# Kernel tuning notes

Hardware: AMD Instinct MI355X
Metric: run time of the kernel (lower is better)

The kernel has to match this reference:

```python
import jax, jax.numpy as jnp
import numpy as np

B, S, D, H = 2, 2048, 1024, 16
DK = D // H
NEG = -1.0e9


def setup_inputs() -> dict:
    key = jax.random.key(0)
    ks = jax.random.split(key, 11)
    inp = {
        "q": jax.random.normal(ks[0], (B, S, D), jnp.float32),
        "k": jax.random.normal(ks[1], (B, S, D), jnp.float32),
        "v": jax.random.normal(ks[2], (B, S, D), jnp.float32),
        "mask": jnp.tril(jnp.ones((S, S), jnp.int32))[None, None],  # causal [1,1,S,S]
    }
    scale = 0.02
    inp["w_q"] = jax.random.normal(ks[3], (D, D), jnp.float32) * scale
    inp["b_q"] = jnp.zeros((D,), jnp.float32)
    inp["w_k"] = jax.random.normal(ks[4], (D, D), jnp.float32) * scale
    inp["b_k"] = jnp.zeros((D,), jnp.float32)
    inp["w_v"] = jax.random.normal(ks[5], (D, D), jnp.float32) * scale
    inp["b_v"] = jnp.zeros((D,), jnp.float32)
    inp["w_o"] = jax.random.normal(ks[6], (D, D), jnp.float32) * scale
    inp["b_o"] = jnp.zeros((D,), jnp.float32)
    return inp


def reference(q, k, v, mask, w_q, b_q, w_k, b_k, w_v, b_v, w_o, b_o):
    # projections: [B,S,D] -> [B,H,S,DK]
    def proj(x, w, b):
        y = jnp.einsum("bsd,de->bse", x, w) + b
        return y.reshape(B, S, H, DK).transpose(0, 2, 1, 3)

    Q = proj(q, w_q, b_q)
    K = proj(k, w_k, b_k)
    V = proj(v, w_v, b_v)
    # explicit scores matrix, faithful to the original naive attention
    scores = jnp.einsum("bhsd,bhtd->bhst", Q, K) / jnp.sqrt(jnp.float32(DK))
    scores = jnp.where(mask == 0, NEG, scores)
    attn = jax.nn.softmax(scores, axis=-1)  # dropout p=0.0 -> identity
    x = jnp.einsum("bhst,bhtd->bhsd", attn, V)
    x = x.transpose(0, 2, 1, 3).reshape(B, S, D)
    return jnp.einsum("bsd,de->bse", x, w_o) + b_o
```

## Files before the change

### kernel.cpp

```cpp
#include <hip/hip_runtime.h>
#include <hip/hip_bf16.h>

typedef __bf16 bf16;
typedef __bf16 bf16x2 __attribute__((ext_vector_type(2)));
typedef __bf16 bf16x8 __attribute__((ext_vector_type(8)));
typedef float f32x4 __attribute__((ext_vector_type(4)));

#define MFMA16(a, b, c) __builtin_amdgcn_mfma_f32_16x16x32_bf16(a, b, c, 0, 0, 0)

#define QSCALE 0.18033688f

__global__ __launch_bounds__(256) void convert_k(const float* __restrict__ q,
                                                 const float* __restrict__ k,
                                                 const float* __restrict__ v,
                                                 bf16* __restrict__ qb,
                                                 bf16* __restrict__ kb,
                                                 bf16* __restrict__ vb) {
  const float* src = blockIdx.y == 0 ? q : blockIdx.y == 1 ? k : v;
  bf16* dst = blockIdx.y == 0 ? qb : blockIdx.y == 1 ? kb : vb;
  const size_t i = ((size_t)blockIdx.x * 256 + threadIdx.x) * 8;
  float4 a = *(const float4*)(src + i);
  float4 b = *(const float4*)(src + i + 4);
  bf16x8 o;
  o[0] = (bf16)a.x; o[1] = (bf16)a.y; o[2] = (bf16)a.z; o[3] = (bf16)a.w;
  o[4] = (bf16)b.x; o[5] = (bf16)b.y; o[6] = (bf16)b.z; o[7] = (bf16)b.w;
  *(bf16x8*)(dst + i) = o;
}

__global__ __launch_bounds__(256) void transpose_w(const float* __restrict__ w0,
                                                   const float* __restrict__ w1,
                                                   const float* __restrict__ w2,
                                                   const float* __restrict__ w3,
                                                   bf16* __restrict__ dst) {
  __shared__ bf16 T[64][68];
  const float* W = blockIdx.z == 0 ? w0 : blockIdx.z == 1 ? w1
                   : blockIdx.z == 2 ? w2 : w3;
  bf16* Y = dst + (size_t)blockIdx.z * 1024 * 1024;
  const int t = threadIdx.x, r = t >> 2, c4 = t & 3;
  const int k0 = blockIdx.y * 64, n0 = blockIdx.x * 64;

  const float4* src = (const float4*)(W + (size_t)(k0 + r) * 1024 + n0 + c4 * 16);
  float4 f0 = src[0], f1 = src[1], f2 = src[2], f3 = src[3];
  bf16* row = &T[r][c4 * 16];
  row[0] = (bf16)f0.x; row[1] = (bf16)f0.y; row[2] = (bf16)f0.z; row[3] = (bf16)f0.w;
  row[4] = (bf16)f1.x; row[5] = (bf16)f1.y; row[6] = (bf16)f1.z; row[7] = (bf16)f1.w;
  row[8] = (bf16)f2.x; row[9] = (bf16)f2.y; row[10] = (bf16)f2.z; row[11] = (bf16)f2.w;
  row[12] = (bf16)f3.x; row[13] = (bf16)f3.y; row[14] = (bf16)f3.z; row[15] = (bf16)f3.w;
  __syncthreads();

  bf16x8 o0, o1;
#pragma unroll
  for (int j = 0; j < 8; ++j) o0[j] = T[c4 * 16 + j][r];
#pragma unroll
  for (int j = 0; j < 8; ++j) o1[j] = T[c4 * 16 + 8 + j][r];
  bf16* d = Y + (size_t)(n0 + r) * 1024 + k0 + c4 * 16;
  *(bf16x8*)d = o0;
  *(bf16x8*)(d + 8) = o1;
}

template <int QKV, int MT>
__global__ __launch_bounds__(256, 3) void gemm_p(
    const bf16* __restrict__ xq, const bf16* __restrict__ xk,
    const bf16* __restrict__ xv, const bf16* __restrict__ Wt,
    const float* __restrict__ bq, const float* __restrict__ bk,
    const float* __restrict__ bv, bf16* __restrict__ Qp,
    bf16* __restrict__ Kp, bf16* __restrict__ Vtp, float* __restrict__ Yf) {
  constexpr int AROWS = MT * 32;
  __shared__ bf16 Al[AROWS * 72];
  __shared__ bf16 Bl[128 * 72];

  const int z = QKV ? blockIdx.z : 0;
  const bf16* X = QKV ? (z == 0 ? xq : z == 1 ? xk : xv) : xq;
  const bf16* Bt = Wt + (size_t)z * 1048576;
  const float* bias = QKV ? (z == 0 ? bq : z == 1 ? bk : bv) : bq;
  const float escale = (QKV && z == 0) ? QSCALE : 1.0f;

  const int t = threadIdx.x;
  const int wave = t >> 6, lane = t & 63, quad = lane >> 4, l16 = lane & 15;
  const int wm = (wave >> 1) * (MT * 16), wn = (wave & 1) * 64;
  const int bm = blockIdx.y * AROWS, bn = blockIdx.x * 128;

  constexpr int NA = (MT == 4) ? 4 : 2;
  const int arow = (MT == 4) ? (t >> 1) : (t >> 2);
  const int acol = (MT == 4) ? ((t & 1) * 32) : ((t & 3) * 16);
  const int brow = t >> 1, bcol = (t & 1) * 32;
  const bf16* gA = X + (size_t)(bm + arow) * 1024 + acol;
  const bf16* gB = Bt + (size_t)(bn + brow) * 1024 + bcol;

  bf16x8 ra[NA], rb[4];
#pragma unroll
  for (int j = 0; j < NA; ++j) ra[j] = *(const bf16x8*)(gA + j * 8);
#pragma unroll
  for (int j = 0; j < 4; ++j) rb[j] = *(const bf16x8*)(gB + j * 8);

  f32x4 acc[MT][4] = {};

  for (int kb = 0; kb < 1024; kb += 64) {
    __syncthreads();
#pragma unroll
    for (int j = 0; j < NA; ++j)
      *(bf16x8*)(Al + arow * 72 + acol + j * 8) = ra[j];
#pragma unroll
    for (int j = 0; j < 4; ++j)
      *(bf16x8*)(Bl + brow * 72 + bcol + j * 8) = rb[j];
    __syncthreads();

    if (kb + 64 < 1024) {
#pragma unroll
      for (int j = 0; j < NA; ++j)
        ra[j] = *(const bf16x8*)(gA + kb + 64 + j * 8);
#pragma unroll
      for (int j = 0; j < 4; ++j)
        rb[j] = *(const bf16x8*)(gB + kb + 64 + j * 8);
    }

#pragma unroll
    for (int kk = 0; kk < 2; ++kk) {
      bf16x8 af[MT], bfr[4];
#pragma unroll
      for (int mt = 0; mt < MT; ++mt)
        af[mt] =
            *(const bf16x8*)(Al + (wm + mt * 16 + l16) * 72 + kk * 32 + quad * 8);
#pragma unroll
      for (int nt = 0; nt < 4; ++nt)
        bfr[nt] =
            *(const bf16x8*)(Bl + (wn + nt * 16 + l16) * 72 + kk * 32 + quad * 8);
#pragma unroll
      for (int mt = 0; mt < MT; ++mt)
#pragma unroll
        for (int nt = 0; nt < 4; ++nt)
          acc[mt][nt] = MFMA16(af[mt], bfr[nt], acc[mt][nt]);
    }
  }

  if (QKV && z == 2) {
    bf16* Tt = Al;
    const int b = bm >> 11;
    __syncthreads();
#pragma unroll
    for (int half = 0; half < 2; ++half) {
      if ((wave & 1) == half) {
#pragma unroll
        for (int nt = 0; nt < 4; ++nt) {
          const int ln = nt * 16 + l16;
          const float bia = bias[bn + half * 64 + ln];
#pragma unroll
          for (int mt = 0; mt < 4; ++mt)
#pragma unroll
            for (int r = 0; r < 4; ++r) {
              const int m = wm + mt * 16 + quad * 4 + r;
              Tt[ln * 136 + m] = (bf16)(acc[mt][nt][r] + bia);
            }
        }
      }
      __syncthreads();
      {
        const int ln = t >> 2, seg = (t & 3) * 32;
        const int gn = bn + half * 64 + ln;
        const int h = gn >> 6, dk = gn & 63;
        const int s0 = (bm & 2047) + seg;
        bf16* dstp = Vtp + ((size_t)(b * 16 + h) * 64 + dk) * 2048 + s0;
        const bf16* srcp = Tt + ln * 136 + seg;
#pragma unroll
        for (int j = 0; j < 4; ++j)
          *(bf16x8*)(dstp + j * 8) = *(const bf16x8*)(srcp + j * 8);
      }
      __syncthreads();
    }
  } else {
#pragma unroll
    for (int mt = 0; mt < MT; ++mt)
#pragma unroll
      for (int nt = 0; nt < 4; ++nt) {
        const int gn = bn + wn + nt * 16 + l16;
        const float bia = bias[gn];
#pragma unroll
        for (int r = 0; r < 4; ++r) {
          const int gm = bm + wm + mt * 16 + quad * 4 + r;
          const float val = (acc[mt][nt][r] + bia) * escale;
          if (!QKV) {
            Yf[(size_t)gm * 1024 + gn] = val;
          } else {
            const int b = gm >> 11, s = gm & 2047;
            const int h = gn >> 6, dk = gn & 63;
            bf16* Y = (z == 0) ? Qp : Kp;
            Y[((size_t)(b * 16 + h) * 2048 + s) * 64 + dk] = (bf16)val;
          }
        }
      }
  }
}

__global__ __launch_bounds__(256) void attn_k(const bf16* __restrict__ Q,
                                              const bf16* __restrict__ K,
                                              const bf16* __restrict__ Vt,
                                              bf16* __restrict__ X) {
  __shared__ bf16 Kl[64 * 72];
  __shared__ bf16 Vl[64 * 72];
  __shared__ bf16 Pb[4][16 * 72];

  const int t = threadIdx.x;
  const int wave = t >> 6, lane = t & 63, quad = lane >> 4, l16 = lane & 15;
  const int pairx = blockIdx.x, bh = blockIdx.y;
  const int b = bh >> 4, h = bh & 15;

  const bf16* Qb = Q + (size_t)bh * 2048 * 64;
  const bf16* Kb = K + (size_t)bh * 2048 * 64;
  const bf16* Vb = Vt + (size_t)bh * 64 * 2048;

  const int srow = t >> 2;
  const int scol = (t & 3) * 16;
  const int crow = (srow & 32) + ((srow & 1) << 4) + ((srow & 31) >> 1);

  bf16x8 onesf;
#pragma unroll
  for (int i = 0; i < 8; ++i) onesf[i] = (bf16)1.0f;

  bf16* Pw = Pb[wave];

  for (int phase = 0; phase < 2; ++phase) {
    const int qtile = phase ? (31 - pairx) : pairx;
    const int ntiles = qtile + 1;
    const int q0 = qtile * 64 + wave * 16;

    bf16x8 qf0 = *(const bf16x8*)(Qb + (q0 + l16) * 64 + quad * 8);
    bf16x8 qf1 = *(const bf16x8*)(Qb + (q0 + l16) * 64 + 32 + quad * 8);

    f32x4 o[4] = {};
    f32x4 o4 = {};

    {
      const bf16* kp = Kb + srow * 64 + scol;
      const bf16* vp = Vb + (size_t)srow * 2048 + scol;
      bf16x8 k0r = *(const bf16x8*)kp;
      bf16x8 k1r = *(const bf16x8*)(kp + 8);
      bf16x8 v0r = *(const bf16x8*)vp;
      bf16x8 v1r = *(const bf16x8*)(vp + 8);
      *(bf16x8*)(Kl + crow * 72 + scol) = k0r;
      *(bf16x8*)(Kl + crow * 72 + scol + 8) = k1r;
      *(bf16x8*)(Vl + srow * 72 + scol) = v0r;
      *(bf16x8*)(Vl + srow * 72 + scol + 8) = v1r;
    }
    __syncthreads();

    for (int kt = 0; kt < ntiles; ++kt) {
      const int k0 = kt * 64;
      const bool more = (kt + 1) < ntiles;
      bf16x8 kr0, kr1, vr0, vr1;
      if (more) {
        const bf16* kp = Kb + (k0 + 64 + srow) * 64 + scol;
        const bf16* vp = Vb + (size_t)srow * 2048 + k0 + 64 + scol;
        kr0 = *(const bf16x8*)kp;
        kr1 = *(const bf16x8*)(kp + 8);
        vr0 = *(const bf16x8*)vp;
        vr1 = *(const bf16x8*)(vp + 8);
      }

      f32x4 sc[4];
#pragma unroll
      for (int nt = 0; nt < 4; ++nt) {
        bf16x8 kf0 = *(const bf16x8*)(Kl + (nt * 16 + l16) * 72 + quad * 8);
        bf16x8 kf1 = *(const bf16x8*)(Kl + (nt * 16 + l16) * 72 + 32 + quad * 8);
        f32x4 s = {};
        s = MFMA16(qf0, kf0, s);
        s = MFMA16(qf1, kf1, s);
        sc[nt] = s;
      }

      const bool interior = (k0 + 63) <= q0;
#pragma unroll
      for (int r = 0; r < 4; ++r) {
        const int row = quad * 4 + r;
        float e0 = exp2f(sc[0][r]);
        float e1 = exp2f(sc[1][r]);
        float e2 = exp2f(sc[2][r]);
        float e3 = exp2f(sc[3][r]);
        if (!interior) {
          const int qg = q0 + row;
          const int key0 = k0 + 2 * l16;
          if (key0 > qg) e0 = 0.f;
          if (key0 + 1 > qg) e1 = 0.f;
          if (key0 + 32 > qg) e2 = 0.f;
          if (key0 + 33 > qg) e3 = 0.f;
        }
        bf16x2 p01, p23;
        p01[0] = (bf16)e0; p01[1] = (bf16)e1;
        p23[0] = (bf16)e2; p23[1] = (bf16)e3;
        *(bf16x2*)(Pw + row * 72 + 2 * l16) = p01;
        *(bf16x2*)(Pw + row * 72 + 32 + 2 * l16) = p23;
      }
      __builtin_amdgcn_s_waitcnt(0xC07F);

      bf16x8 pf0 = *(const bf16x8*)(Pw + l16 * 72 + quad * 8);
      bf16x8 pf1 = *(const bf16x8*)(Pw + l16 * 72 + 32 + quad * 8);
      o4 = MFMA16(pf0, onesf, o4);
      o4 = MFMA16(pf1, onesf, o4);
#pragma unroll
      for (int dt = 0; dt < 4; ++dt) {
        bf16x8 vf0 = *(const bf16x8*)(Vl + (dt * 16 + l16) * 72 + quad * 8);
        bf16x8 vf1 = *(const bf16x8*)(Vl + (dt * 16 + l16) * 72 + 32 + quad * 8);
        o[dt] = MFMA16(pf0, vf0, o[dt]);
        o[dt] = MFMA16(pf1, vf1, o[dt]);
      }

      __syncthreads();
      if (more) {
        *(bf16x8*)(Kl + crow * 72 + scol) = kr0;
        *(bf16x8*)(Kl + crow * 72 + scol + 8) = kr1;
        *(bf16x8*)(Vl + srow * 72 + scol) = vr0;
        *(bf16x8*)(Vl + srow * 72 + scol + 8) = vr1;
        __syncthreads();
      }
    }

#pragma unroll
    for (int r = 0; r < 4; ++r) {
      const float rinv = 1.0f / o4[r];
      const int qg = q0 + quad * 4 + r;
#pragma unroll
      for (int dt = 0; dt < 4; ++dt) {
        const int col = h * 64 + dt * 16 + l16;
        X[((size_t)b * 2048 + qg) * 1024 + col] = (bf16)(o[dt][r] * rinv);
      }
    }
    __syncthreads();
  }
}

extern "C" void kernel_launch(void* const* d_in, const int* in_sizes, int n_in,
                              void* d_out, int out_size, void* d_ws,
                              size_t ws_size, hipStream_t stream) {
  const float* q = (const float*)d_in[0];
  const float* k = (const float*)d_in[1];
  const float* v = (const float*)d_in[2];
  const float* w_q = (const float*)d_in[4];
  const float* b_q = (const float*)d_in[5];
  const float* w_k = (const float*)d_in[6];
  const float* b_k = (const float*)d_in[7];
  const float* w_v = (const float*)d_in[8];
  const float* b_v = (const float*)d_in[9];
  const float* w_o = (const float*)d_in[10];
  const float* b_o = (const float*)d_in[11];

  bf16* ws = (bf16*)d_ws;
  const size_t NELEM = (size_t)4096 * 1024;
  bf16* Qp = ws;
  bf16* Kp = ws + NELEM;
  bf16* Vtp = ws + 2 * NELEM;
  bf16* Xp = ws + 3 * NELEM;
  bf16* Wt = ws + 4 * NELEM;
  bf16* Wto = Wt + 3145728;
  bf16* qb = Xp;
  bf16* kb = (bf16*)d_out;
  bf16* vb = kb + NELEM;

  convert_k<<<dim3(2048, 3), 256, 0, stream>>>(q, k, v, qb, kb, vb);
  transpose_w<<<dim3(16, 16, 4), 256, 0, stream>>>(w_q, w_k, w_v, w_o, Wt);

  gemm_p<1, 4><<<dim3(8, 32, 3), 256, 0, stream>>>(
      qb, kb, vb, Wt, b_q, b_k, b_v, Qp, Kp, Vtp, nullptr);
  attn_k<<<dim3(16, 32), 256, 0, stream>>>(Qp, Kp, Vtp, Xp);
  gemm_p<0, 2><<<dim3(8, 64), 256, 0, stream>>>(
      Xp, nullptr, nullptr, Wto, b_o, nullptr, nullptr, nullptr, nullptr,
      nullptr, (float*)d_out);
}
```

Before: 244.3 us.

## Rewrite attention kernel with 32x32 MFMA, double-buffered swizzled LDS, register softmax

The attention kernel now gives each wave 32 query rows (128-row block tiles) and uses 32x32x16 bf16 MFMA with a transposed S=K*Q^T so P can be built in registers through cross-half shuffles. This replaces the LDS round-trip for P and the ones-vector MFMA used for row sums. K/V tiles are double-buffered in XOR-swizzled LDS so each iteration needs only one barrier. A 1D grid maps heads across XCDs and pairs short and long causal tiles for balance, with setprio around MFMA bursts. The costs are higher register pressure from two f32x16 accumulators and coarser causal tiles that do more masked work on the diagonal.

```diff
diff --git a/kernel.cpp b/kernel.cpp
--- a/kernel.cpp
+++ b/kernel.cpp
@@ -5,8 +5,10 @@
 typedef __bf16 bf16x2 __attribute__((ext_vector_type(2)));
 typedef __bf16 bf16x8 __attribute__((ext_vector_type(8)));
 typedef float f32x4 __attribute__((ext_vector_type(4)));
+typedef float f32x16 __attribute__((ext_vector_type(16)));
 
 #define MFMA16(a, b, c) __builtin_amdgcn_mfma_f32_16x16x32_bf16(a, b, c, 0, 0, 0)
+#define MFMA32(a, b, c) __builtin_amdgcn_mfma_f32_32x32x16_bf16(a, b, c, 0, 0, 0)
 
 #define QSCALE 0.18033688f
 
@@ -191,139 +193,165 @@
   }
 }
 
-__global__ __launch_bounds__(256) void attn_k(const bf16* __restrict__ Q,
-                                              const bf16* __restrict__ K,
-                                              const bf16* __restrict__ Vt,
-                                              bf16* __restrict__ X) {
-  __shared__ bf16 Kl[64 * 72];
-  __shared__ bf16 Vl[64 * 72];
-  __shared__ bf16 Pb[4][16 * 72];
+__global__ __launch_bounds__(256, 2) void attn_k(const bf16* __restrict__ Q,
+                                                 const bf16* __restrict__ K,
+                                                 const bf16* __restrict__ Vt,
+                                                 bf16* __restrict__ X) {
+  __shared__ __align__(16) bf16 Kl[2][64 * 64];
+  __shared__ __align__(16) bf16 Vl[2][64 * 64];
+  __shared__ float rsL[4][32];
 
   const int t = threadIdx.x;
-  const int wave = t >> 6, lane = t & 63, quad = lane >> 4, l16 = lane & 15;
-  const int pairx = blockIdx.x, bh = blockIdx.y;
-  const int b = bh >> 4, h = bh & 15;
+  const int wave = t >> 6, lane = t & 63;
+  const int cl = lane & 31, h = lane >> 5;
+
+  const int n = blockIdx.x;
+  const int xcd = n & 7, mm = n >> 3;
+  const int bh = xcd + 8 * (mm & 3);
+  const int ii = mm >> 2;
+  const int qt = (ii < 8) ? ii : 23 - ii;
+  const int ntiles = 2 * qt + 2;
+  const int q0 = qt * 128 + wave * 32;
+  const int b = bh >> 4, hh = bh & 15;
 
   const bf16* Qb = Q + (size_t)bh * 2048 * 64;
   const bf16* Kb = K + (size_t)bh * 2048 * 64;
   const bf16* Vb = Vt + (size_t)bh * 64 * 2048;
 
-  const int srow = t >> 2;
-  const int scol = (t & 3) * 16;
-  const int crow = (srow & 32) + ((srow & 1) << 4) + ((srow & 31) >> 1);
-
-  bf16x8 onesf;
-#pragma unroll
-  for (int i = 0; i < 8; ++i) onesf[i] = (bf16)1.0f;
-
-  bf16* Pw = Pb[wave];
-
-  for (int phase = 0; phase < 2; ++phase) {
-    const int qtile = phase ? (31 - pairx) : pairx;
-    const int ntiles = qtile + 1;
-    const int q0 = qtile * 64 + wave * 16;
-
-    bf16x8 qf0 = *(const bf16x8*)(Qb + (q0 + l16) * 64 + quad * 8);
-    bf16x8 qf1 = *(const bf16x8*)(Qb + (q0 + l16) * 64 + 32 + quad * 8);
-
-    f32x4 o[4] = {};
-    f32x4 o4 = {};
-
-    {
-      const bf16* kp = Kb + srow * 64 + scol;
-      const bf16* vp = Vb + (size_t)srow * 2048 + scol;
-      bf16x8 k0r = *(const bf16x8*)kp;
-      bf16x8 k1r = *(const bf16x8*)(kp + 8);
-      bf16x8 v0r = *(const bf16x8*)vp;
-      bf16x8 v1r = *(const bf16x8*)(vp + 8);
-      *(bf16x8*)(Kl + crow * 72 + scol) = k0r;
-      *(bf16x8*)(Kl + crow * 72 + scol + 8) = k1r;
-      *(bf16x8*)(Vl + srow * 72 + scol) = v0r;
-      *(bf16x8*)(Vl + srow * 72 + scol + 8) = v1r;
+  bf16x8 qf[4];
+#pragma unroll
+  for (int ks = 0; ks < 4; ++ks)
+    qf[ks] = *(const bf16x8*)(Qb + (size_t)(q0 + cl) * 64 + ks * 16 + h * 8);
+
+  const int sr = t >> 2, sc4 = t & 3;
+  const int swz = (sr & 7) << 4;
+  const int d0 = sr * 128 + ((sc4 * 32) ^ swz);
+  const int d1 = sr * 128 + ((sc4 * 32 + 16) ^ swz);
+  const bf16* gK = Kb + sr * 64 + sc4 * 16;
+  const bf16* gV = Vb + (size_t)sr * 2048 + sc4 * 16;
+
+  const int fswz = (cl & 7) << 4;
+
+  f32x16 o0 = {}, o1 = {};
+  float rs = 0.f;
+
+  {
+    bf16x8 ka = *(const bf16x8*)gK;
+    bf16x8 kb2 = *(const bf16x8*)(gK + 8);
+    bf16x8 va = *(const bf16x8*)gV;
+    bf16x8 vb2 = *(const bf16x8*)(gV + 8);
+    *(bf16x8*)((char*)Kl[0] + d0) = ka;
+    *(bf16x8*)((char*)Kl[0] + d1) = kb2;
+    *(bf16x8*)((char*)Vl[0] + d0) = va;
+    *(bf16x8*)((char*)Vl[0] + d1) = vb2;
+  }
+  __syncthreads();
+
+  for (int kt = 0; kt < ntiles; ++kt) {
+    const int cur = kt & 1;
+    const int k0 = kt * 64;
+    const bool more = kt + 1 < ntiles;
+    bf16x8 ka, kb2, va, vb2;
+    if (more) {
+      const bf16* nK = gK + (size_t)(kt + 1) * 4096;
+      const bf16* nV = gV + (kt + 1) * 64;
+      ka = *(const bf16x8*)nK;
+      kb2 = *(const bf16x8*)(nK + 8);
+      va = *(const bf16x8*)nV;
+      vb2 = *(const bf16x8*)(nV + 8);
+    }
+
+    f32x16 s0 = {}, s1 = {};
+    const char* Kc = (const char*)Kl[cur];
+    __builtin_amdgcn_s_setprio(1);
+#pragma unroll
+    for (int ks = 0; ks < 4; ++ks) {
+      const int cb = ks * 32 + h * 16;
+      bf16x8 f0 = *(const bf16x8*)(Kc + cl * 128 + (cb ^ fswz));
+      bf16x8 f1 = *(const bf16x8*)(Kc + (cl + 32) * 128 + (cb ^ fswz));
+      s0 = MFMA32(f0, qf[ks], s0);
+      s1 = MFMA32(f1, qf[ks], s1);
+    }
+    __builtin_amdgcn_s_setprio(0);
+
+    const bool interior = (k0 + 63) <= q0;
+    unsigned pk[8][2];
+    float ts = 0.f;
+    auto smax = [&](const f32x16& s, int mk) {
+#pragma unroll
+      for (int sl = 0; sl < 4; ++sl)
+#pragma unroll
+        for (int p = 0; p < 2; ++p) {
+          float e0 = exp2f(s[sl * 4 + 2 * p]);
+          float e1 = exp2f(s[sl * 4 + 2 * p + 1]);
+          if (!interior) {
+            const int ky = k0 + mk * 32 + 8 * sl + 4 * h + 2 * p;
+            const int qg = q0 + cl;
+            if (ky > qg) e0 = 0.f;
+            if (ky + 1 > qg) e1 = 0.f;
+          }
+          ts += e0 + e1;
+          union { bf16x2 v; unsigned u; } cv;
+          cv.v[0] = (bf16)e0;
+          cv.v[1] = (bf16)e1;
+          pk[mk * 4 + sl][p] = cv.u;
+        }
+    };
+    smax(s0, 0);
+    smax(s1, 1);
+    rs += ts;
+
+    bf16x8 pf[4];
+#pragma unroll
+    for (int ks = 0; ks < 4; ++ks) {
+      const unsigned oe0 = pk[2 * ks][0], oe1 = pk[2 * ks][1];
+      const unsigned oo0 = pk[2 * ks + 1][0], oo1 = pk[2 * ks + 1][1];
+      const unsigned pe0 = (unsigned)__shfl_xor((int)oe0, 32, 64);
+      const unsigned pe1 = (unsigned)__shfl_xor((int)oe1, 32, 64);
+      const unsigned po0 = (unsigned)__shfl_xor((int)oo0, 32, 64);
+      const unsigned po1 = (unsigned)__shfl_xor((int)oo1, 32, 64);
+      union { unsigned u[4]; bf16x8 v; } fu;
+      fu.u[0] = h ? po0 : oe0;
+      fu.u[1] = h ? po1 : oe1;
+      fu.u[2] = h ? oo0 : pe0;
+      fu.u[3] = h ? oo1 : pe1;
+      pf[ks] = fu.v;
+    }
+
+    const char* Vc = (const char*)Vl[cur];
+    __builtin_amdgcn_s_setprio(1);
+#pragma unroll
+    for (int ks = 0; ks < 4; ++ks) {
+      const int cb = ks * 32 + h * 16;
+      bf16x8 v0f = *(const bf16x8*)(Vc + cl * 128 + (cb ^ fswz));
+      bf16x8 v1f = *(const bf16x8*)(Vc + (cl + 32) * 128 + (cb ^ fswz));
+      o0 = MFMA32(pf[ks], v0f, o0);
+      o1 = MFMA32(pf[ks], v1f, o1);
+    }
+    __builtin_amdgcn_s_setprio(0);
+
+    if (more) {
+      char* Kd = (char*)Kl[cur ^ 1];
+      char* Vd = (char*)Vl[cur ^ 1];
+      *(bf16x8*)(Kd + d0) = ka;
+      *(bf16x8*)(Kd + d1) = kb2;
+      *(bf16x8*)(Vd + d0) = va;
+      *(bf16x8*)(Vd + d1) = vb2;
     }
     __syncthreads();
-
-    for (int kt = 0; kt < ntiles; ++kt) {
-      const int k0 = kt * 64;
-      const bool more = (kt + 1) < ntiles;
-      bf16x8 kr0, kr1, vr0, vr1;
-      if (more) {
-        const bf16* kp = Kb + (k0 + 64 + srow) * 64 + scol;
-        const bf16* vp = Vb + (size_t)srow * 2048 + k0 + 64 + scol;
-        kr0 = *(const bf16x8*)kp;
-        kr1 = *(const bf16x8*)(kp + 8);
-        vr0 = *(const bf16x8*)vp;
-        vr1 = *(const bf16x8*)(vp + 8);
-      }
-
-      f32x4 sc[4];
-#pragma unroll
-      for (int nt = 0; nt < 4; ++nt) {
-        bf16x8 kf0 = *(const bf16x8*)(Kl + (nt * 16 + l16) * 72 + quad * 8);
-        bf16x8 kf1 = *(const bf16x8*)(Kl + (nt * 16 + l16) * 72 + 32 + quad * 8);
-        f32x4 s = {};
-        s = MFMA16(qf0, kf0, s);
-        s = MFMA16(qf1, kf1, s);
-        sc[nt] = s;
-      }
-
-      const bool interior = (k0 + 63) <= q0;
-#pragma unroll
-      for (int r = 0; r < 4; ++r) {
-        const int row = quad * 4 + r;
-        float e0 = exp2f(sc[0][r]);
-        float e1 = exp2f(sc[1][r]);
-        float e2 = exp2f(sc[2][r]);
-        float e3 = exp2f(sc[3][r]);
-        if (!interior) {
-          const int qg = q0 + row;
-          const int key0 = k0 + 2 * l16;
-          if (key0 > qg) e0 = 0.f;
-          if (key0 + 1 > qg) e1 = 0.f;
-          if (key0 + 32 > qg) e2 = 0.f;
-          if (key0 + 33 > qg) e3 = 0.f;
-        }
-        bf16x2 p01, p23;
-        p01[0] = (bf16)e0; p01[1] = (bf16)e1;
-        p23[0] = (bf16)e2; p23[1] = (bf16)e3;
-        *(bf16x2*)(Pw + row * 72 + 2 * l16) = p01;
-        *(bf16x2*)(Pw + row * 72 + 32 + 2 * l16) = p23;
-      }
-      __builtin_amdgcn_s_waitcnt(0xC07F);
-
-      bf16x8 pf0 = *(const bf16x8*)(Pw + l16 * 72 + quad * 8);
-      bf16x8 pf1 = *(const bf16x8*)(Pw + l16 * 72 + 32 + quad * 8);
-      o4 = MFMA16(pf0, onesf, o4);
-      o4 = MFMA16(pf1, onesf, o4);
-#pragma unroll
-      for (int dt = 0; dt < 4; ++dt) {
-        bf16x8 vf0 = *(const bf16x8*)(Vl + (dt * 16 + l16) * 72 + quad * 8);
-        bf16x8 vf1 = *(const bf16x8*)(Vl + (dt * 16 + l16) * 72 + 32 + quad * 8);
-        o[dt] = MFMA16(pf0, vf0, o[dt]);
-        o[dt] = MFMA16(pf1, vf1, o[dt]);
-      }
-
-      __syncthreads();
-      if (more) {
-        *(bf16x8*)(Kl + crow * 72 + scol) = kr0;
-        *(bf16x8*)(Kl + crow * 72 + scol + 8) = kr1;
-        *(bf16x8*)(Vl + srow * 72 + scol) = vr0;
-        *(bf16x8*)(Vl + srow * 72 + scol + 8) = vr1;
-        __syncthreads();
-      }
-    }
-
-#pragma unroll
-    for (int r = 0; r < 4; ++r) {
-      const float rinv = 1.0f / o4[r];
-      const int qg = q0 + quad * 4 + r;
-#pragma unroll
-      for (int dt = 0; dt < 4; ++dt) {
-        const int col = h * 64 + dt * 16 + l16;
-        X[((size_t)b * 2048 + qg) * 1024 + col] = (bf16)(o[dt][r] * rinv);
-      }
-    }
-    __syncthreads();
+  }
+
+  const float rtot = rs + __shfl_xor(rs, 32, 64);
+  rsL[wave][cl] = 1.0f / rtot;
+  __builtin_amdgcn_s_waitcnt(0xC07F);
+  bf16* Xb = X + (size_t)b * 2048 * 1024 + hh * 64;
+#pragma unroll
+  for (int g = 0; g < 16; ++g) {
+    const int qr = (g & 3) + 8 * (g >> 2) + 4 * h;
+    const float ri = rsL[wave][qr];
+    const int qg = q0 + qr;
+    Xb[(size_t)qg * 1024 + cl] = (bf16)(o0[g] * ri);
+    Xb[(size_t)qg * 1024 + 32 + cl] = (bf16)(o1[g] * ri);
   }
 }
 
@@ -359,7 +387,7 @@
 
   gemm_p<1, 4><<<dim3(8, 32, 3), 256, 0, stream>>>(
       qb, kb, vb, Wt, b_q, b_k, b_v, Qp, Kp, Vtp, nullptr);
-  attn_k<<<dim3(16, 32), 256, 0, stream>>>(Qp, Kp, Vtp, Xp);
+  attn_k<<<dim3(512), 256, 0, stream>>>(Qp, Kp, Vtp, Xp);
   gemm_p<0, 2><<<dim3(8, 64), 256, 0, stream>>>(
       Xp, nullptr, nullptr, Wto, b_o, nullptr, nullptr, nullptr, nullptr,
       nullptr, (float*)d_out);
```

Result: no change. 248.7 us (+1.8%).
